# Kernel tuning notes

Hardware: AMD Instinct MI355X
Metric: run time of the kernel (lower is better)

The kernel has to match this reference:

```python
import jax, jax.numpy as jnp
import numpy as np

B, C, H, W = 4, 512, 64, 64
CA = C // 2  # attention hidden channels


def _conv1x1(x, w):
    # w: [O, I], x: [B, I, H, W]
    return jnp.einsum('oi,bihw->bohw', w, x)


def _conv3x3(x, w, b):
    y = jax.lax.conv_general_dilated(x, w, (1, 1), 'SAME',
                                     dimension_numbers=('NCHW', 'OIHW', 'NCHW'))
    return y + b[None, :, None, None]


def _scan_dir(x, w, b, axis, reverse):
    # IRNN recurrence along `axis`: prev = relu(prev * w + b + x_t), per-channel w,b.
    # The boundary position (first in scan order after un-flipping) stays zero,
    # matching the torch code which never writes it.
    xs = jnp.moveaxis(x, axis, 0)          # [L, B, C, other]
    if reverse:
        xs = xs[::-1]
    wb = w.reshape(1, -1, 1)
    bb = b.reshape(1, -1, 1)

    def step(prev, xt):
        new = jax.nn.relu(prev * wb + bb + xt)
        return new, new

    init = jax.nn.relu(xs[0])
    _, ys = jax.lax.scan(step, init, xs[1:])
    ys = jnp.concatenate([jnp.zeros_like(ys[:1]), ys], axis=0)
    if reverse:
        ys = ys[::-1]
    return jnp.moveaxis(ys, 0, axis)


def _irnn(x, wu, wr, wd, wl, bu, br, bd, bl):
    up = _scan_dir(x, wu, bu, 2, True)     # scans from bottom row upward
    right = _scan_dir(x, wr, br, 3, False)
    down = _scan_dir(x, wd, bd, 2, False)
    left = _scan_dir(x, wl, bl, 3, True)
    return up, right, down, left


def setup_inputs() -> dict:
    key = jax.random.key(0)
    ks = jax.random.split(key, 32)

    def n(k, shape, scale):
        return jax.random.normal(k, shape, jnp.float32) * scale

    inp = {
        'x': n(ks[0], (B, C, H, W), 1.0),
        # Attention: conv3x3(C->C/2)+b, conv3x3(C/2->C/2)+b, conv1x1(C/2->4)+b
        'a_w1': n(ks[1], (CA, C, 3, 3), (C * 9) ** -0.5),
        'a_b1': n(ks[2], (CA,), 0.02),
        'a_w2': n(ks[3], (CA, CA, 3, 3), (CA * 9) ** -0.5),
        'a_b2': n(ks[4], (CA,), 0.02),
        'a_w3': n(ks[5], (4, CA, 1, 1), CA ** -0.5),
        'a_b3': n(ks[6], (4,), 0.02),
        'cin_w': n(ks[7], (C, C), C ** -0.5),   # conv_in 1x1, bias=False
        'c2_w': n(ks[8], (C, 4 * C), (4 * C) ** -0.5),
        'c3_w': n(ks[9], (C, 4 * C), (4 * C) ** -0.5),
    }
    # IRNN per-channel recurrence weights (alpha=1.0 init) and biases
    i = 10
    for tag in ('i1', 'i2'):
        for d in ('u', 'r', 'd', 'l'):
            inp[f'{tag}_w{d}'] = jnp.ones((C,), jnp.float32)
            inp[f'{tag}_b{d}'] = n(ks[i], (C,), 0.05)
            i += 1
    return inp


def reference(x, a_w1, a_b1, a_w2, a_b2, a_w3, a_b3, cin_w,
              i1_wu, i1_bu, i1_wr, i1_br, i1_wd, i1_bd, i1_wl, i1_bl,
              c2_w,
              i2_wu, i2_bu, i2_wr, i2_br, i2_wd, i2_bd, i2_wl, i2_bl,
              c3_w):
    # Attention branch — computed but NEVER applied: the original torch code
    # uses out-of-place .mul() and discards the result (faithful reproduction).
    a = jax.nn.relu(_conv3x3(x, a_w1, a_b1))
    a = jax.nn.relu(_conv3x3(a, a_w2, a_b2))
    _weight = jax.nn.sigmoid(_conv1x1(a, a_w3[:, :, 0, 0]) + a_b3[None, :, None, None])

    out = _conv1x1(x, cin_w)
    u, r, d, l = _irnn(out, i1_wu, i1_wr, i1_wd, i1_wl, i1_bu, i1_br, i1_bd, i1_bl)
    out = jnp.concatenate([u, r, d, l], axis=1)   # [B, 4C, H, W]
    out = _conv1x1(out, c2_w)
    u, r, d, l = _irnn(out, i2_wu, i2_wr, i2_wd, i2_wl, i2_bu, i2_br, i2_bd, i2_bl)
    out = jnp.concatenate([u, r, d, l], axis=1)
    out = jax.nn.relu(_conv1x1(out, c3_w))
    return out
```

## Files before the change

### kernel.cpp

```cpp
#include <hip/hip_runtime.h>
#include <stdint.h>

#define NB 4
#define CB 512
#define HH 64
#define WW 64
#define HW 4096
#define C4 2048
#define PTOT (NB*HW)

typedef float  f32x4  __attribute__((ext_vector_type(4)));
typedef short  bf16x8 __attribute__((ext_vector_type(8)));

__device__ __forceinline__ float relu_f(float v){ return v > 0.f ? v : 0.f; }

__device__ __forceinline__ float bf2f(unsigned short u){
    union { uint32_t i; float f; } v; v.i = ((uint32_t)u) << 16; return v.f;
}
__device__ __forceinline__ unsigned short f2bf(float f){
    union { float f; uint32_t i; } v; v.f = f;
    uint32_t r = v.i + 0x7FFFu + ((v.i >> 16) & 1u);
    return (unsigned short)(r >> 16);
}

__device__ __forceinline__ void gload16(const void* g, void* l){
    __builtin_amdgcn_global_load_lds(
        (const __attribute__((address_space(1))) uint32_t*)g,
        (__attribute__((address_space(3))) uint32_t*)l, 16, 0, 0);
}

__global__ __launch_bounds__(256) void prep_fused(
    const float* __restrict__ x, unsigned short* __restrict__ xT,
    const float* __restrict__ a, unsigned short* __restrict__ oa,
    const float* __restrict__ b, unsigned short* __restrict__ ob,
    const float* __restrict__ c, unsigned short* __restrict__ oc)
{
    const int t = threadIdx.x;
    if (blockIdx.x >= 2048) {
        int i = (blockIdx.x - 2048) * 256 + t;
        const float* src; unsigned short* dst; int j;
        if (i < 65536)        { src = a; dst = oa; j = i; }
        else if (i < 327680)  { src = b; dst = ob; j = i - 65536; }
        else                  { src = c; dst = oc; j = i - 327680; }
        float4 v = ((const float4*)src)[j];
        ushort4 o;
        o.x = f2bf(v.x); o.y = f2bf(v.y); o.z = f2bf(v.z); o.w = f2bf(v.w);
        ((ushort4*)dst)[j] = o;
        return;
    }
    __shared__ unsigned short tile[64][72];
    const int tb = blockIdx.x;
    const int p0 = (tb & 63) * 64;
    const int c0 = ((tb >> 6) & 7) * 64;
    const int bb = tb >> 9;

    const int pl = (t & 15) * 4;
    const int cl = t >> 4;
    const float* src = x + ((size_t)bb * CB + c0) * HW + p0;
    #pragma unroll
    for (int r = 0; r < 4; r++) {
        int c2 = cl + r * 16;
        float4 v = *(const float4*)(src + (size_t)c2 * HW + pl);
        tile[pl + 0][c2] = f2bf(v.x);
        tile[pl + 1][c2] = f2bf(v.y);
        tile[pl + 2][c2] = f2bf(v.z);
        tile[pl + 3][c2] = f2bf(v.w);
    }
    __syncthreads();
    unsigned short* dst = xT + ((size_t)bb * HW + p0) * CB + c0;
    const int cl2 = (t & 15) * 4;
    const int pl2 = t >> 4;
    #pragma unroll
    for (int r = 0; r < 4; r++) {
        int p = pl2 + r * 16;
        ushort4 o = *(ushort4*)&tile[p][cl2];
        *(ushort4*)(dst + (size_t)p * CB + cl2) = o;
    }
}

template<int K, int OUTMODE>
__global__ __launch_bounds__(256) void gemm_cl(
    const unsigned short* __restrict__ A,
    const unsigned short* __restrict__ Bw,
    void* __restrict__ out)
{
    __shared__ __align__(16) char lds[81920];

    const int t    = threadIdx.x;
    const int lane = t & 63;
    const int wid  = t >> 6;
    const int p0   = blockIdx.x * 128;
    const int o0   = blockIdx.y * 128;

    const int l15 = lane & 15;
    const int l4  = lane >> 4;
    const int wp  = (wid & 1) * 64;
    const int wo  = (wid >> 1) * 64;
    const int rowA = wp + l15;
    const int rowB = wo + l15;
    const int swzA = (rowA & 7) << 4;
    const int swzB = (rowB & 7) << 4;

    f32x4 acc[4][4];
    #pragma unroll
    for (int m = 0; m < 4; m++)
        #pragma unroll
        for (int n = 0; n < 4; n++) acc[m][n] = (f32x4)0.f;

    const int srow  = t >> 3;
    const int scolb = (t & 7) * 16;

    auto A_STAGE = [&](int k0, int aoff) {
        #pragma unroll
        for (int q = 0; q < 4; q++) {
            const int row = q * 32 + srow;
            const int kk  = k0 + ((scolb ^ ((row & 7) << 4)) >> 1);
            gload16(A + (size_t)(p0 + row) * K + kk,
                    lds + aoff + q * 4096 + wid * 1024);
        }
    };
    auto B_STAGE = [&](int k0, int boff) {
        #pragma unroll
        for (int q = 0; q < 4; q++) {
            const int row = q * 32 + srow;
            const int kk  = k0 + ((scolb ^ ((row & 7) << 4)) >> 1);
            gload16(Bw + (size_t)(o0 + row) * K + kk,
                    lds + boff + q * 4096 + wid * 1024);
        }
    };
    auto COMPUTE = [&](int aoff, int boff) {
        const char* cA = lds + aoff;
        const char* cB = lds + boff;
        #pragma unroll
        for (int kh = 0; kh < 2; kh++) {
            const int colb = kh * 64 + l4 * 16;
            bf16x8 a[4], b[4];
            #pragma unroll
            for (int m = 0; m < 4; m++)
                a[m] = *(const bf16x8*)(cA + (rowA + m * 16) * 128 + (colb ^ swzA));
            #pragma unroll
            for (int n = 0; n < 4; n++)
                b[n] = *(const bf16x8*)(cB + (rowB + n * 16) * 128 + (colb ^ swzB));
            __builtin_amdgcn_s_setprio(1);
            #pragma unroll
            for (int m = 0; m < 4; m++)
                #pragma unroll
                for (int n = 0; n < 4; n++)
                    acc[m][n] = __builtin_amdgcn_mfma_f32_16x16x32_bf16(
                                    a[m], b[n], acc[m][n], 0, 0, 0);
            __builtin_amdgcn_s_setprio(0);
        }
    };

    const int NT = K / 64;
    int aC = 0, aN = 16384, aF = 32768;

    A_STAGE(0, aC);
    B_STAGE(0, 49152);
    A_STAGE(64, aN);

    #pragma unroll 1
    for (int tt = 0; tt < NT; ++tt) {
        const int bC = 49152 + ((tt & 1) << 14);
        const int bN = 49152 + (((tt + 1) & 1) << 14);
        if (tt + 1 < NT) B_STAGE((tt + 1) * 64, bN);
        if (tt + 2 < NT) A_STAGE((tt + 2) * 64, aF);

        if (tt + 2 < NT)      asm volatile("s_waitcnt vmcnt(12)" ::: "memory");
        else if (tt + 1 < NT) asm volatile("s_waitcnt vmcnt(8)"  ::: "memory");
        else                  asm volatile("s_waitcnt vmcnt(0)"  ::: "memory");
        __builtin_amdgcn_s_barrier();
        __builtin_amdgcn_sched_barrier(0);

        COMPUTE(aC, bC);
        __builtin_amdgcn_s_barrier();

        const int tmp = aC; aC = aN; aN = aF; aF = tmp;
    }

    if (OUTMODE == 0) {
        unsigned short* op = (unsigned short*)out;
        #pragma unroll
        for (int m = 0; m < 4; m++)
            #pragma unroll
            for (int r = 0; r < 4; r++) {
                const int p = p0 + wp + m * 16 + l4 * 4 + r;
                #pragma unroll
                for (int n = 0; n < 4; n++) {
                    const int o = wo + n * 16 + l15 + o0;
                    op[(size_t)p * CB + o] = f2bf(acc[m][n][r]);
                }
            }
    } else {
        __syncthreads();
        float (*tl)[132] = (float(*)[132])lds;
        const int bb   = p0 >> 12;
        const int phw0 = p0 & (HW - 1);
        #pragma unroll
        for (int half = 0; half < 2; half++) {
            if ((wid >> 1) == half) {
                #pragma unroll
                for (int n = 0; n < 4; n++)
                    #pragma unroll
                    for (int m = 0; m < 4; m++)
                        #pragma unroll
                        for (int r = 0; r < 4; r++)
                            tl[n * 16 + l15][wp + m * 16 + l4 * 4 + r] = acc[m][n][r];
            }
            __syncthreads();
            const int orow = t >> 2;
            const int pseg = (t & 3) * 32;
            float* dst = (float*)out +
                ((size_t)(bb * CB + o0 + half * 64 + orow)) * HW + phw0 + pseg;
            #pragma unroll
            for (int j = 0; j < 8; j++) {
                float4 v = *(float4*)&tl[orow][pseg + j * 4];
                v.x = relu_f(v.x); v.y = relu_f(v.y); v.z = relu_f(v.z); v.w = relu_f(v.w);
                *(float4*)(dst + j * 4) = v;
            }
            __syncthreads();
        }
    }
}

__global__ __launch_bounds__(256) void irnn_fused(
    const unsigned short* __restrict__ in, unsigned short* __restrict__ outc,
    const float* __restrict__ wu, const float* __restrict__ bu,
    const float* __restrict__ wr, const float* __restrict__ br,
    const float* __restrict__ wd, const float* __restrict__ bd,
    const float* __restrict__ wl, const float* __restrict__ bl)
{
    const int dir = blockIdx.y;
    const float* wv; const float* bv; int pstep, rev;
    if      (dir == 0) { wv = wu; bv = bu; pstep = 64; rev = 1; }
    else if (dir == 1) { wv = wr; bv = br; pstep = 1;  rev = 0; }
    else if (dir == 2) { wv = wd; bv = bd; pstep = 64; rev = 0; }
    else               { wv = wl; bv = bl; pstep = 1;  rev = 1; }
    const int dirOff = dir * 512;

    const int idx = blockIdx.x * 256 + threadIdx.x;
    const int c = idx & 511;
    const int f = (idx >> 9) & 63;
    const int b = idx >> 15;
    const int fbase = (pstep == 64) ? f : f * 64;

    const float wc = wv[c], bc = bv[c];
    const int t0 = rev ? 63 : 0;
    const int dp = rev ? -pstep : pstep;
    const int istep = dp * CB;
    const int ostep = dp * C4;

    const unsigned short* ip = in   + ((size_t)b * HW + fbase + (size_t)t0 * pstep) * CB + c;
    unsigned short*       op = outc + ((size_t)b * HW + fbase + (size_t)t0 * pstep) * C4 + dirOff + c;

    float s = relu_f(bf2f(ip[0]));
    op[0] = 0;

    unsigned short v0 = ip[1*istep], v1 = ip[2*istep], v2 = ip[3*istep], v3 = ip[4*istep],
                   v4 = ip[5*istep], v5 = ip[6*istep], v6 = ip[7*istep], v7 = ip[8*istep];

#define DO(kk, vv) { s = relu_f(fmaf(s, wc, bc + bf2f(vv))); op[(kk)*ostep] = f2bf(s); }
    for (int g = 0; g < 6; ++g) {
        const int k0 = 1 + 8 * g;
        DO(k0+0, v0); v0 = ip[(k0+ 8)*istep];
        DO(k0+1, v1); v1 = ip[(k0+ 9)*istep];
        DO(k0+2, v2); v2 = ip[(k0+10)*istep];
        DO(k0+3, v3); v3 = ip[(k0+11)*istep];
        DO(k0+4, v4); v4 = ip[(k0+12)*istep];
        DO(k0+5, v5); v5 = ip[(k0+13)*istep];
        DO(k0+6, v6); v6 = ip[(k0+14)*istep];
        DO(k0+7, v7); v7 = ip[(k0+15)*istep];
    }
    DO(49, v0); v0 = ip[57*istep];
    DO(50, v1); v1 = ip[58*istep];
    DO(51, v2); v2 = ip[59*istep];
    DO(52, v3); v3 = ip[60*istep];
    DO(53, v4); v4 = ip[61*istep];
    DO(54, v5); v5 = ip[62*istep];
    DO(55, v6); v6 = ip[63*istep];
    DO(56, v7);
    DO(57, v0); DO(58, v1); DO(59, v2); DO(60, v3);
    DO(61, v4); DO(62, v5); DO(63, v6);
#undef DO
}

extern "C" void kernel_launch(void* const* d_in, const int* in_sizes, int n_in,
                              void* d_out, int out_size, void* d_ws, size_t ws_size,
                              hipStream_t stream) {
    const float* x     = (const float*)d_in[0];
    const float* cin_w = (const float*)d_in[7];
    const float* c2_w  = (const float*)d_in[8];
    const float* c3_w  = (const float*)d_in[9];
    const float* i1_wu = (const float*)d_in[10];
    const float* i1_bu = (const float*)d_in[11];
    const float* i1_wr = (const float*)d_in[12];
    const float* i1_br = (const float*)d_in[13];
    const float* i1_wd = (const float*)d_in[14];
    const float* i1_bd = (const float*)d_in[15];
    const float* i1_wl = (const float*)d_in[16];
    const float* i1_bl = (const float*)d_in[17];
    const float* i2_wu = (const float*)d_in[18];
    const float* i2_bu = (const float*)d_in[19];
    const float* i2_wr = (const float*)d_in[20];
    const float* i2_br = (const float*)d_in[21];
    const float* i2_wd = (const float*)d_in[22];
    const float* i2_bd = (const float*)d_in[23];
    const float* i2_wl = (const float*)d_in[24];
    const float* i2_bl = (const float*)d_in[25];

    char* ws = (char*)d_ws;
    unsigned short* xT     = (unsigned short*)(ws);
    unsigned short* concat = (unsigned short*)(ws + (size_t)16 * 1024 * 1024);
    unsigned short* mid    = (unsigned short*)(ws + (size_t)80 * 1024 * 1024);
    unsigned short* wA     = (unsigned short*)(ws + (size_t)96 * 1024 * 1024);
    unsigned short* wB     = (unsigned short*)(wA + 512 * 512);
    unsigned short* wC     = (unsigned short*)(wB + 512 * 2048);

    prep_fused<<<4352, 256, 0, stream>>>(x, xT, cin_w, wA, c2_w, wB, c3_w, wC);

    dim3 ggrid(PTOT/128, 4);
    dim3 sgrid(512, 4);

    gemm_cl<512, 0><<<ggrid, 256, 0, stream>>>(xT, wA, mid);

    irnn_fused<<<sgrid, 256, 0, stream>>>(mid, concat,
        i1_wu, i1_bu, i1_wr, i1_br, i1_wd, i1_bd, i1_wl, i1_bl);

    gemm_cl<2048, 0><<<ggrid, 256, 0, stream>>>(concat, wB, mid);

    irnn_fused<<<sgrid, 256, 0, stream>>>(mid, concat,
        i2_wu, i2_bu, i2_wr, i2_br, i2_wd, i2_bd, i2_wl, i2_bl);

    gemm_cl<2048, 1><<<ggrid, 256, 0, stream>>>(concat, wC, d_out);
}
```

Before: 142.5 us.

## Load GEMM B operand directly into registers and shrink LDS pipeline

The B (weight) tile is no longer staged through shared memory. Each wave now loads its B fragments straight from global memory into double-buffered registers. The A pipeline drops from triple to double buffering, which cuts LDS use from 80KB to about 33KB so more blocks can be resident per CU. The costs are higher register pressure, redundant global reads of B across waves, and a shallower prefetch depth for A.

```diff
diff --git a/kernel.cpp b/kernel.cpp
--- a/kernel.cpp
+++ b/kernel.cpp
@@ -84,7 +84,7 @@
     const unsigned short* __restrict__ Bw,
     void* __restrict__ out)
 {
-    __shared__ __align__(16) char lds[81920];
+    __shared__ __align__(16) char lds[34048];
 
     const int t    = threadIdx.x;
     const int lane = t & 63;
@@ -97,9 +97,7 @@
     const int wp  = (wid & 1) * 64;
     const int wo  = (wid >> 1) * 64;
     const int rowA = wp + l15;
-    const int rowB = wo + l15;
     const int swzA = (rowA & 7) << 4;
-    const int swzB = (rowB & 7) << 4;
 
     f32x4 acc[4][4];
     #pragma unroll
@@ -119,63 +117,58 @@
                     lds + aoff + q * 4096 + wid * 1024);
         }
     };
-    auto B_STAGE = [&](int k0, int boff) {
-        #pragma unroll
-        for (int q = 0; q < 4; q++) {
-            const int row = q * 32 + srow;
-            const int kk  = k0 + ((scolb ^ ((row & 7) << 4)) >> 1);
-            gload16(Bw + (size_t)(o0 + row) * K + kk,
-                    lds + boff + q * 4096 + wid * 1024);
-        }
+
+    const unsigned short* bptr = Bw + (size_t)(o0 + wo + l15) * K + l4 * 8;
+    auto B_LOAD = [&](int k0, bf16x8 (&bs)[8]) {
+        #pragma unroll
+        for (int kh = 0; kh < 2; kh++)
+            #pragma unroll
+            for (int n = 0; n < 4; n++)
+                bs[kh * 4 + n] = *(const bf16x8*)(bptr + (size_t)n * (16 * K)
+                                                  + k0 + kh * 32);
     };
-    auto COMPUTE = [&](int aoff, int boff) {
-        const char* cA = lds + aoff;
-        const char* cB = lds + boff;
+
+    auto COMPUTE = [&](int aoff, const bf16x8 (&bs)[8]) {
         #pragma unroll
         for (int kh = 0; kh < 2; kh++) {
             const int colb = kh * 64 + l4 * 16;
-            bf16x8 a[4], b[4];
+            bf16x8 a[4];
             #pragma unroll
             for (int m = 0; m < 4; m++)
-                a[m] = *(const bf16x8*)(cA + (rowA + m * 16) * 128 + (colb ^ swzA));
-            #pragma unroll
-            for (int n = 0; n < 4; n++)
-                b[n] = *(const bf16x8*)(cB + (rowB + n * 16) * 128 + (colb ^ swzB));
+                a[m] = *(const bf16x8*)(lds + aoff + (rowA + m * 16) * 128
+                                        + (colb ^ swzA));
             __builtin_amdgcn_s_setprio(1);
             #pragma unroll
             for (int m = 0; m < 4; m++)
                 #pragma unroll
                 for (int n = 0; n < 4; n++)
                     acc[m][n] = __builtin_amdgcn_mfma_f32_16x16x32_bf16(
-                                    a[m], b[n], acc[m][n], 0, 0, 0);
+                                    a[m], bs[kh * 4 + n], acc[m][n], 0, 0, 0);
             __builtin_amdgcn_s_setprio(0);
         }
     };
 
     const int NT = K / 64;
-    int aC = 0, aN = 16384, aF = 32768;
-
-    A_STAGE(0, aC);
-    B_STAGE(0, 49152);
-    A_STAGE(64, aN);
-
-    #pragma unroll 1
-    for (int tt = 0; tt < NT; ++tt) {
-        const int bC = 49152 + ((tt & 1) << 14);
-        const int bN = 49152 + (((tt + 1) & 1) << 14);
-        if (tt + 1 < NT) B_STAGE((tt + 1) * 64, bN);
-        if (tt + 2 < NT) A_STAGE((tt + 2) * 64, aF);
-
-        if (tt + 2 < NT)      asm volatile("s_waitcnt vmcnt(12)" ::: "memory");
-        else if (tt + 1 < NT) asm volatile("s_waitcnt vmcnt(8)"  ::: "memory");
-        else                  asm volatile("s_waitcnt vmcnt(0)"  ::: "memory");
+    bf16x8 bX[8], bY[8];
+
+    A_STAGE(0, 0);
+    B_LOAD(0, bX);
+
+    auto TILE = [&](int tt, int cur, int nxt, bf16x8 (&bcur)[8], bf16x8 (&bnxt)[8]) {
+        const bool more = (tt + 1 < NT);
+        if (more) { A_STAGE((tt + 1) * 64, nxt); B_LOAD((tt + 1) * 64, bnxt); }
+        if (more) asm volatile("s_waitcnt vmcnt(12)" ::: "memory");
+        else      asm volatile("s_waitcnt vmcnt(0)"  ::: "memory");
         __builtin_amdgcn_s_barrier();
         __builtin_amdgcn_sched_barrier(0);
-
-        COMPUTE(aC, bC);
+        COMPUTE(cur, bcur);
         __builtin_amdgcn_s_barrier();
-
-        const int tmp = aC; aC = aN; aN = aF; aF = tmp;
+    };
+
+    #pragma unroll 1
+    for (int tp = 0; tp < NT; tp += 2) {
+        TILE(tp,     0,     16384, bX, bY);
+        TILE(tp + 1, 16384, 0,     bY, bX);
     }
 
     if (OUTMODE == 0) {
```

After: 224.9 us. 1.58x slower.

## Widen GEMM tile to 128x256 with plain double-buffered LDS staging

Applied to the files above, without the earlier changes.

The GEMM block tile grows from 128x128 to 128x256 outputs, so each wave holds 64x128 accumulators, A tiles are reused across more outputs and the grid halves in the output dimension. The old triple-buffered A / double-buffered B prefetch is replaced by a simpler double buffer that stages A and B together one step ahead, and the setprio hints are removed. This aims to cut global and LDS traffic per FLOP, at the cost of doubling accumulator registers (lower occupancy), fewer blocks (256x2=512) and a shallower prefetch pipeline.

```diff
diff --git a/kernel.cpp b/kernel.cpp
--- a/kernel.cpp
+++ b/kernel.cpp
@@ -84,98 +84,84 @@
     const unsigned short* __restrict__ Bw,
     void* __restrict__ out)
 {
-    __shared__ __align__(16) char lds[81920];
+    __shared__ __align__(16) char lds[98304];
 
     const int t    = threadIdx.x;
     const int lane = t & 63;
     const int wid  = t >> 6;
     const int p0   = blockIdx.x * 128;
-    const int o0   = blockIdx.y * 128;
+    const int o0   = blockIdx.y * 256;
 
     const int l15 = lane & 15;
     const int l4  = lane >> 4;
-    const int wp  = (wid & 1) * 64;
-    const int wo  = (wid >> 1) * 64;
-    const int rowA = wp + l15;
-    const int rowB = wo + l15;
-    const int swzA = (rowA & 7) << 4;
-    const int swzB = (rowB & 7) << 4;
-
-    f32x4 acc[4][4];
+    const int wm  = (wid >> 1) * 64;
+    const int wn  = (wid & 1) * 128;
+    const int rowA = wm + l15;
+    const int swz  = (l15 & 7) << 4;
+
+    f32x4 acc[4][8];
     #pragma unroll
     for (int m = 0; m < 4; m++)
         #pragma unroll
-        for (int n = 0; n < 4; n++) acc[m][n] = (f32x4)0.f;
+        for (int n = 0; n < 8; n++) acc[m][n] = (f32x4)0.f;
 
     const int srow  = t >> 3;
     const int scolb = (t & 7) * 16;
 
-    auto A_STAGE = [&](int k0, int aoff) {
+    auto STAGE = [&](int k0, int off) {
         #pragma unroll
         for (int q = 0; q < 4; q++) {
             const int row = q * 32 + srow;
             const int kk  = k0 + ((scolb ^ ((row & 7) << 4)) >> 1);
             gload16(A + (size_t)(p0 + row) * K + kk,
-                    lds + aoff + q * 4096 + wid * 1024);
-        }
-    };
-    auto B_STAGE = [&](int k0, int boff) {
-        #pragma unroll
-        for (int q = 0; q < 4; q++) {
+                    lds + off + q * 4096 + wid * 1024);
+        }
+        #pragma unroll
+        for (int q = 0; q < 8; q++) {
             const int row = q * 32 + srow;
             const int kk  = k0 + ((scolb ^ ((row & 7) << 4)) >> 1);
             gload16(Bw + (size_t)(o0 + row) * K + kk,
-                    lds + boff + q * 4096 + wid * 1024);
+                    lds + off + 16384 + q * 4096 + wid * 1024);
         }
     };
-    auto COMPUTE = [&](int aoff, int boff) {
-        const char* cA = lds + aoff;
-        const char* cB = lds + boff;
+    auto COMPUTE = [&](int off) {
+        const char* cA = lds + off;
+        const char* cB = lds + off + 16384;
         #pragma unroll
         for (int kh = 0; kh < 2; kh++) {
             const int colb = kh * 64 + l4 * 16;
-            bf16x8 a[4], b[4];
+            bf16x8 a[4], b[8];
             #pragma unroll
             for (int m = 0; m < 4; m++)
-                a[m] = *(const bf16x8*)(cA + (rowA + m * 16) * 128 + (colb ^ swzA));
-            #pragma unroll
-            for (int n = 0; n < 4; n++)
-                b[n] = *(const bf16x8*)(cB + (rowB + n * 16) * 128 + (colb ^ swzB));
-            __builtin_amdgcn_s_setprio(1);
+                a[m] = *(const bf16x8*)(cA + (rowA + m * 16) * 128 + (colb ^ swz));
+            #pragma unroll
+            for (int n = 0; n < 8; n++)
+                b[n] = *(const bf16x8*)(cB + (wn + n * 16 + l15) * 128 + (colb ^ swz));
             #pragma unroll
             for (int m = 0; m < 4; m++)
                 #pragma unroll
-                for (int n = 0; n < 4; n++)
+                for (int n = 0; n < 8; n++)
                     acc[m][n] = __builtin_amdgcn_mfma_f32_16x16x32_bf16(
                                     a[m], b[n], acc[m][n], 0, 0, 0);
-            __builtin_amdgcn_s_setprio(0);
         }
     };
 
     const int NT = K / 64;
-    int aC = 0, aN = 16384, aF = 32768;
-
-    A_STAGE(0, aC);
-    B_STAGE(0, 49152);
-    A_STAGE(64, aN);
-
+    STAGE(0, 0);
     #pragma unroll 1
     for (int tt = 0; tt < NT; ++tt) {
-        const int bC = 49152 + ((tt & 1) << 14);
-        const int bN = 49152 + (((tt + 1) & 1) << 14);
-        if (tt + 1 < NT) B_STAGE((tt + 1) * 64, bN);
-        if (tt + 2 < NT) A_STAGE((tt + 2) * 64, aF);
-
-        if (tt + 2 < NT)      asm volatile("s_waitcnt vmcnt(12)" ::: "memory");
-        else if (tt + 1 < NT) asm volatile("s_waitcnt vmcnt(8)"  ::: "memory");
-        else                  asm volatile("s_waitcnt vmcnt(0)"  ::: "memory");
+        const int cur = (tt & 1) * 49152;
+        const int nxt = 49152 - cur;
+        if (tt + 1 < NT) {
+            STAGE((tt + 1) * 64, nxt);
+            asm volatile("s_waitcnt vmcnt(12)" ::: "memory");
+        } else {
+            asm volatile("s_waitcnt vmcnt(0)" ::: "memory");
+        }
         __builtin_amdgcn_s_barrier();
         __builtin_amdgcn_sched_barrier(0);
-
-        COMPUTE(aC, bC);
+        COMPUTE(cur);
         __builtin_amdgcn_s_barrier();
-
-        const int tmp = aC; aC = aN; aN = aF; aF = tmp;
     }
 
     if (OUTMODE == 0) {
@@ -184,10 +170,10 @@
         for (int m = 0; m < 4; m++)
             #pragma unroll
             for (int r = 0; r < 4; r++) {
-                const int p = p0 + wp + m * 16 + l4 * 4 + r;
+                const int p = p0 + wm + m * 16 + l4 * 4 + r;
                 #pragma unroll
-                for (int n = 0; n < 4; n++) {
-                    const int o = wo + n * 16 + l15 + o0;
+                for (int n = 0; n < 8; n++) {
+                    const int o = o0 + wn + n * 16 + l15;
                     op[(size_t)p * CB + o] = f2bf(acc[m][n][r]);
                 }
             }
@@ -197,21 +183,23 @@
         const int bb   = p0 >> 12;
         const int phw0 = p0 & (HW - 1);
         #pragma unroll
-        for (int half = 0; half < 2; half++) {
-            if ((wid >> 1) == half) {
+        for (int h = 0; h < 4; h++) {
+            if ((wid & 1) == (h >> 1)) {
                 #pragma unroll
-                for (int n = 0; n < 4; n++)
+                for (int n4 = 0; n4 < 4; n4++) {
+                    const int n = (h & 1) * 4 + n4;
                     #pragma unroll
                     for (int m = 0; m < 4; m++)
                         #pragma unroll
                         for (int r = 0; r < 4; r++)
-                            tl[n * 16 + l15][wp + m * 16 + l4 * 4 + r] = acc[m][n][r];
+                            tl[n4 * 16 + l15][wm + m * 16 + l4 * 4 + r] = acc[m][n][r];
+                }
             }
             __syncthreads();
             const int orow = t >> 2;
             const int pseg = (t & 3) * 32;
             float* dst = (float*)out +
-                ((size_t)(bb * CB + o0 + half * 64 + orow)) * HW + phw0 + pseg;
+                ((size_t)(bb * CB + o0 + h * 64 + orow)) * HW + phw0 + pseg;
             #pragma unroll
             for (int j = 0; j < 8; j++) {
                 float4 v = *(float4*)&tl[orow][pseg + j * 4];
@@ -318,7 +306,7 @@
 
     prep_fused<<<4352, 256, 0, stream>>>(x, xT, cin_w, wA, c2_w, wB, c3_w, wC);
 
-    dim3 ggrid(PTOT/128, 4);
+    dim3 ggrid(PTOT/128, CB/256);
     dim3 sgrid(512, 4);
 
     gemm_cl<512, 0><<<ggrid, 256, 0, stream>>>(xT, wA, mid);
```

New measurement: 150.5 us. 1.06x slower.
